# Optimization experiments

Hardware: AMD Instinct MI355X
Metric: run time of the kernel (lower is better)

Reference implementation:

```python
import jax, jax.numpy as jnp
import numpy as np

MU = 0.25  # commitment weight

def setup_inputs() -> dict:
    key = jax.random.key(0)
    k1, k2 = jax.random.split(key)
    x = jax.random.normal(k1, (32, 4096, 32), dtype=jnp.float32)
    codebook = jax.random.normal(k2, (256, 32), dtype=jnp.float32)
    return {"x": x, "codebook": codebook}

def reference(x, codebook):
    B, T, D = x.shape
    K = codebook.shape[0]
    xf = x.reshape(-1, D)  # [N, D]
    d2 = (jnp.sum(xf * xf, axis=-1, keepdims=True)
          + jnp.sum(codebook * codebook, axis=-1)[None, :]
          - 2.0 * (xf @ codebook.T))
    logits = -d2
    probs = jax.nn.softmax(logits, axis=-1)          # [N, K]
    indices = jnp.argmax(logits, axis=-1)            # [N]
    quants_hard = codebook[indices]                  # gather [N, D]
    commitment = jnp.mean((jax.lax.stop_gradient(quants_hard) - xf) ** 2, axis=-1)
    codebook_loss = jnp.mean((quants_hard - jax.lax.stop_gradient(xf)) ** 2, axis=-1)
    loss = codebook_loss + MU * commitment           # [N]
    quants = jax.lax.stop_gradient(quants_hard - xf) + xf  # straight-through
    return (indices.reshape(B, T),
            probs.reshape(B, T, K),
            quants.reshape(B, T, D),
            loss.reshape(B, T))
```

## Files before the change

kernel.cpp:

```cpp
#include <hip/hip_runtime.h>
#include <math.h>

constexpr int D   = 32;
constexpr int K   = 256;
constexpr int RPW = 32;
constexpr int WPB = 4;
constexpr int RPB = RPW * WPB;

typedef __attribute__((ext_vector_type(4))) float fvec4;

template <int CTRL, int RM, int BM>
__device__ __forceinline__ int dpp_i(int id, int v) {
    return __builtin_amdgcn_update_dpp(id, v, CTRL, RM, BM, false);
}

__device__ __forceinline__ float wred_max_f32(float v) {
    const int ID = 0xFF800000;
    v = fmaxf(v, __int_as_float(dpp_i<0x111, 0xF, 0xF>(ID, __float_as_int(v))));
    v = fmaxf(v, __int_as_float(dpp_i<0x112, 0xF, 0xF>(ID, __float_as_int(v))));
    v = fmaxf(v, __int_as_float(dpp_i<0x114, 0xF, 0xF>(ID, __float_as_int(v))));
    v = fmaxf(v, __int_as_float(dpp_i<0x118, 0xF, 0xF>(ID, __float_as_int(v))));
    v = fmaxf(v, __int_as_float(dpp_i<0x142, 0xA, 0xF>(ID, __float_as_int(v))));
    v = fmaxf(v, __int_as_float(dpp_i<0x143, 0xC, 0xF>(ID, __float_as_int(v))));
    return v;
}
__device__ __forceinline__ float wred_add_f32(float v) {
    v = v + __int_as_float(dpp_i<0x111, 0xF, 0xF>(0, __float_as_int(v)));
    v = v + __int_as_float(dpp_i<0x112, 0xF, 0xF>(0, __float_as_int(v)));
    v = v + __int_as_float(dpp_i<0x114, 0xF, 0xF>(0, __float_as_int(v)));
    v = v + __int_as_float(dpp_i<0x118, 0xF, 0xF>(0, __float_as_int(v)));
    v = v + __int_as_float(dpp_i<0x142, 0xA, 0xF>(0, __float_as_int(v)));
    v = v + __int_as_float(dpp_i<0x143, 0xC, 0xF>(0, __float_as_int(v)));
    return v;
}
__device__ __forceinline__ unsigned wred_min_u32(unsigned v) {
    const int ID = (int)0xFFFFFFFF;
    unsigned f;
    f = (unsigned)dpp_i<0x111, 0xF, 0xF>(ID, (int)v); v = v < f ? v : f;
    f = (unsigned)dpp_i<0x112, 0xF, 0xF>(ID, (int)v); v = v < f ? v : f;
    f = (unsigned)dpp_i<0x114, 0xF, 0xF>(ID, (int)v); v = v < f ? v : f;
    f = (unsigned)dpp_i<0x118, 0xF, 0xF>(ID, (int)v); v = v < f ? v : f;
    f = (unsigned)dpp_i<0x142, 0xA, 0xF>(ID, (int)v); v = v < f ? v : f;
    f = (unsigned)dpp_i<0x143, 0xC, 0xF>(ID, (int)v); v = v < f ? v : f;
    return v;
}
__device__ __forceinline__ float bcast63_f32(float v) {
    return __int_as_float(__builtin_amdgcn_readlane(__float_as_int(v), 63));
}

__global__ __launch_bounds__(256, 2) void vq_kernel(
    const float* __restrict__ x,
    const float* __restrict__ cb,
    float* __restrict__ o_idx,
    float* __restrict__ o_probs,
    float* __restrict__ o_quants,
    float* __restrict__ o_loss)
{
    const int tid = threadIdx.x;
    const int l   = tid & 63;
    const int wu  = __builtin_amdgcn_readfirstlane(tid >> 6);
    const int wbase = blockIdx.x * RPB + wu * RPW;

    float cr[4][D];
    #pragma unroll
    for (int j = 0; j < 4; ++j) {
        const float4* cp = reinterpret_cast<const float4*>(cb) + (size_t)(l * 4 + j) * (D / 4);
        #pragma unroll
        for (int i = 0; i < D / 4; ++i) {
            float4 v = cp[i];
            cr[j][4 * i + 0] = v.x; cr[j][4 * i + 1] = v.y;
            cr[j][4 * i + 2] = v.z; cr[j][4 * i + 3] = v.w;
        }
    }
    float ncn[4];
    #pragma unroll
    for (int j = 0; j < 4; ++j) {
        float a0 = 0.f, a1 = 0.f, a2 = 0.f, a3 = 0.f;
        #pragma unroll
        for (int d = 0; d < D; d += 4) {
            a0 += cr[j][d]     * cr[j][d];     a1 += cr[j][d + 1] * cr[j][d + 1];
            a2 += cr[j][d + 2] * cr[j][d + 2]; a3 += cr[j][d + 3] * cr[j][d + 3];
        }
        ncn[j] = -((a0 + a1) + (a2 + a3));
    }

    float xnh;
    {
        const float4* xp = reinterpret_cast<const float4*>(x)
                         + (size_t)(wbase + (l >> 1)) * (D / 4) + (l & 1) * 4;
        float a = 0.f;
        #pragma unroll
        for (int i = 0; i < 4; ++i) {
            float4 v = xp[i];
            a += v.x * v.x + v.y * v.y + v.z * v.z + v.w * v.w;
        }
        float b = __int_as_float(dpp_i<0xB1, 0xF, 0xF>(0, __float_as_int(a)));
        xnh = a + b;
    }

    float    lossv = 0.f, fidx = 0.f;
    unsigned gpark = 0;
    const unsigned codebase = (unsigned)(l * 4);

    for (int g = 0; g < RPW / 8; ++g) {
        float4 vx = reinterpret_cast<const float4*>(x)[(size_t)(wbase + g * 8) * (D / 4) + l];

        #pragma unroll
        for (int rr = 0; rr < 8; ++rr) {
            const int r32 = g * 8 + rr;

            float a0 = 0.f, a1 = 0.f, a2 = 0.f, a3 = 0.f;
            #pragma unroll
            for (int d = 0; d < D; ++d) {
                const int lane = rr * 8 + (d >> 2);
                const int c = d & 3;
                int sb = (c == 0) ? __float_as_int(vx.x)
                       : (c == 1) ? __float_as_int(vx.y)
                       : (c == 2) ? __float_as_int(vx.z)
                       :            __float_as_int(vx.w);
                float xs = __int_as_float(__builtin_amdgcn_readlane(sb, lane));
                a0 = fmaf(cr[0][d], xs, a0);
                a1 = fmaf(cr[1][d], xs, a1);
                a2 = fmaf(cr[2][d], xs, a2);
                a3 = fmaf(cr[3][d], xs, a3);
            }
            float lg0 = fmaf(a0, 2.0f, ncn[0]);
            float lg1 = fmaf(a1, 2.0f, ncn[1]);
            float lg2 = fmaf(a2, 2.0f, ncn[2]);
            float lg3 = fmaf(a3, 2.0f, ncn[3]);

            float m = fmaxf(fmaxf(lg0, lg1), fmaxf(lg2, lg3));
            float gm = bcast63_f32(wred_max_f32(m));

            unsigned c0 = (lg0 == gm) ? (codebase + 0) : 0xFFFFFFFFu;
            unsigned c1 = (lg1 == gm) ? (codebase + 1) : 0xFFFFFFFFu;
            unsigned c2 = (lg2 == gm) ? (codebase + 2) : 0xFFFFFFFFu;
            unsigned c3 = (lg3 == gm) ? (codebase + 3) : 0xFFFFFFFFu;
            unsigned cm = min(min(c0, c1), min(c2, c3));
            unsigned gi = (unsigned)__builtin_amdgcn_readlane((int)wred_min_u32(cm), 63) & 255u;

            float e0 = __expf(lg0 - gm), e1 = __expf(lg1 - gm);
            float e2 = __expf(lg2 - gm), e3 = __expf(lg3 - gm);
            float es = (e0 + e1) + (e2 + e3);
            float ws = wred_add_f32(es);
            float rs = bcast63_f32(__builtin_amdgcn_rcpf(ws));

            fvec4 p4 = { e0 * rs, e1 * rs, e2 * rs, e3 * rs };
            fvec4* pp = reinterpret_cast<fvec4*>(o_probs + (size_t)(wbase + r32) * K) + l;
            __builtin_nontemporal_store(p4, pp);

            bool mA = ((l >> 1) == r32);
            float lv = (xnh - gm) * 0.0390625f;
            lossv = mA ? lv : lossv;
            fidx  = mA ? (float)gi : fidx;
            gpark = ((unsigned)l == (unsigned)r32) ? gi : gpark;
        }
    }

    {
        const int r = l >> 1;
        if ((l & 1) == 0) o_loss[wbase + r] = lossv;
        else              o_idx [wbase + r] = fidx;
    }
    {
        int gsel = __builtin_amdgcn_ds_bpermute((l >> 1) * 4, (int)gpark);
        unsigned gq = (unsigned)gsel & 255u;
        const float4* qs = reinterpret_cast<const float4*>(cb) + (size_t)gq * (D / 4) + (l & 1) * 4;
        float* qd = o_quants + (size_t)(wbase + (l >> 1)) * D + (l & 1) * 16;
        #pragma unroll
        for (int i = 0; i < 4; ++i) {
            float4 v = qs[i];
            fvec4 vv = { v.x, v.y, v.z, v.w };
            __builtin_nontemporal_store(vv, reinterpret_cast<fvec4*>(qd) + i);
        }
    }
}

extern "C" void kernel_launch(void* const* d_in, const int* in_sizes, int n_in,
                              void* d_out, int out_size, void* d_ws, size_t ws_size,
                              hipStream_t stream) {
    const float* x  = (const float*)d_in[0];
    const float* cb = (const float*)d_in[1];
    const int N = in_sizes[0] / D;

    float* out      = (float*)d_out;
    float* o_idx    = out;
    float* o_probs  = o_idx + N;
    float* o_quants = o_probs + (size_t)N * K;
    float* o_loss   = o_quants + (size_t)N * D;

    const int grid = N / RPB;
    vq_kernel<<<grid, 256, 0, stream>>>(x, cb, o_idx, o_probs, o_quants, o_loss);
}
```

Measured before the change: 198.7 us.

## Stage x rows in LDS, use exp2 with prescaled logits, raise occupancy

Each block now copies its 128 input rows into shared memory, and each row's values are read from LDS as broadcast float4 loads instead of through per-element readlane from registers. Logits are prescaled by log2(e) so the softmax can use the hardware exp2 directly, and the loss rescales by ln2. Launch bounds now ask for 3 blocks per CU instead of 2, which tightens the register budget for the 128-float codebook tile each thread keeps. Trade-offs are 16 KB of LDS per block, a block-wide barrier, and a risk of register spills.

```diff
diff --git a/kernel.cpp b/kernel.cpp
--- a/kernel.cpp
+++ b/kernel.cpp
@@ -48,7 +48,7 @@
     return __int_as_float(__builtin_amdgcn_readlane(__float_as_int(v), 63));
 }
 
-__global__ __launch_bounds__(256, 2) void vq_kernel(
+__global__ __launch_bounds__(256, 3) void vq_kernel(
     const float* __restrict__ x,
     const float* __restrict__ cb,
     float* __restrict__ o_idx,
@@ -56,11 +56,22 @@
     float* __restrict__ o_quants,
     float* __restrict__ o_loss)
 {
+    __shared__ float4 xlds[RPB * (D / 4)];
+
     const int tid = threadIdx.x;
     const int l   = tid & 63;
     const int wu  = __builtin_amdgcn_readfirstlane(tid >> 6);
     const int wbase = blockIdx.x * RPB + wu * RPW;
 
+    {
+        const float4* xg = reinterpret_cast<const float4*>(x)
+                         + (size_t)blockIdx.x * RPB * (D / 4);
+        #pragma unroll
+        for (int i = 0; i < 4; ++i) xlds[tid + i * 256] = xg[tid + i * 256];
+    }
+
+    constexpr float SC     = 1.4426950408889634f;
+    constexpr float TWO_SC = 2.8853900817779268f;
     float cr[4][D];
     #pragma unroll
     for (int j = 0; j < 4; ++j) {
@@ -81,7 +92,7 @@
             a0 += cr[j][d]     * cr[j][d];     a1 += cr[j][d + 1] * cr[j][d + 1];
             a2 += cr[j][d + 2] * cr[j][d + 2]; a3 += cr[j][d + 3] * cr[j][d + 3];
         }
-        ncn[j] = -((a0 + a1) + (a2 + a3));
+        ncn[j] = -((a0 + a1) + (a2 + a3)) * SC;
     }
 
     float xnh;
@@ -98,63 +109,60 @@
         xnh = a + b;
     }
 
+    __syncthreads();
+
     float    lossv = 0.f, fidx = 0.f;
     unsigned gpark = 0;
     const unsigned codebase = (unsigned)(l * 4);
-
-    for (int g = 0; g < RPW / 8; ++g) {
-        float4 vx = reinterpret_cast<const float4*>(x)[(size_t)(wbase + g * 8) * (D / 4) + l];
-
-        #pragma unroll
-        for (int rr = 0; rr < 8; ++rr) {
-            const int r32 = g * 8 + rr;
-
-            float a0 = 0.f, a1 = 0.f, a2 = 0.f, a3 = 0.f;
+    const float4* xw4 = xlds + wu * RPW * (D / 4);
+
+    for (int r = 0; r < RPW; ++r) {
+        float a0 = 0.f, a1 = 0.f, a2 = 0.f, a3 = 0.f;
+        #pragma unroll
+        for (int q = 0; q < D / 4; ++q) {
+            float4 xv = xw4[r * (D / 4) + q];
             #pragma unroll
-            for (int d = 0; d < D; ++d) {
-                const int lane = rr * 8 + (d >> 2);
-                const int c = d & 3;
-                int sb = (c == 0) ? __float_as_int(vx.x)
-                       : (c == 1) ? __float_as_int(vx.y)
-                       : (c == 2) ? __float_as_int(vx.z)
-                       :            __float_as_int(vx.w);
-                float xs = __int_as_float(__builtin_amdgcn_readlane(sb, lane));
+            for (int c = 0; c < 4; ++c) {
+                const int d = q * 4 + c;
+                const float xs = (&xv.x)[c];
                 a0 = fmaf(cr[0][d], xs, a0);
                 a1 = fmaf(cr[1][d], xs, a1);
                 a2 = fmaf(cr[2][d], xs, a2);
                 a3 = fmaf(cr[3][d], xs, a3);
             }
-            float lg0 = fmaf(a0, 2.0f, ncn[0]);
-            float lg1 = fmaf(a1, 2.0f, ncn[1]);
-            float lg2 = fmaf(a2, 2.0f, ncn[2]);
-            float lg3 = fmaf(a3, 2.0f, ncn[3]);
-
-            float m = fmaxf(fmaxf(lg0, lg1), fmaxf(lg2, lg3));
-            float gm = bcast63_f32(wred_max_f32(m));
-
-            unsigned c0 = (lg0 == gm) ? (codebase + 0) : 0xFFFFFFFFu;
-            unsigned c1 = (lg1 == gm) ? (codebase + 1) : 0xFFFFFFFFu;
-            unsigned c2 = (lg2 == gm) ? (codebase + 2) : 0xFFFFFFFFu;
-            unsigned c3 = (lg3 == gm) ? (codebase + 3) : 0xFFFFFFFFu;
-            unsigned cm = min(min(c0, c1), min(c2, c3));
-            unsigned gi = (unsigned)__builtin_amdgcn_readlane((int)wred_min_u32(cm), 63) & 255u;
-
-            float e0 = __expf(lg0 - gm), e1 = __expf(lg1 - gm);
-            float e2 = __expf(lg2 - gm), e3 = __expf(lg3 - gm);
-            float es = (e0 + e1) + (e2 + e3);
-            float ws = wred_add_f32(es);
-            float rs = bcast63_f32(__builtin_amdgcn_rcpf(ws));
-
-            fvec4 p4 = { e0 * rs, e1 * rs, e2 * rs, e3 * rs };
-            fvec4* pp = reinterpret_cast<fvec4*>(o_probs + (size_t)(wbase + r32) * K) + l;
-            __builtin_nontemporal_store(p4, pp);
-
-            bool mA = ((l >> 1) == r32);
-            float lv = (xnh - gm) * 0.0390625f;
-            lossv = mA ? lv : lossv;
-            fidx  = mA ? (float)gi : fidx;
-            gpark = ((unsigned)l == (unsigned)r32) ? gi : gpark;
-        }
+        }
+        float slg0 = fmaf(a0, TWO_SC, ncn[0]);
+        float slg1 = fmaf(a1, TWO_SC, ncn[1]);
+        float slg2 = fmaf(a2, TWO_SC, ncn[2]);
+        float slg3 = fmaf(a3, TWO_SC, ncn[3]);
+
+        float m = fmaxf(fmaxf(slg0, slg1), fmaxf(slg2, slg3));
+        float gm = bcast63_f32(wred_max_f32(m));
+
+        unsigned c0 = (slg0 == gm) ? (codebase + 0) : 0xFFFFFFFFu;
+        unsigned c1 = (slg1 == gm) ? (codebase + 1) : 0xFFFFFFFFu;
+        unsigned c2 = (slg2 == gm) ? (codebase + 2) : 0xFFFFFFFFu;
+        unsigned c3 = (slg3 == gm) ? (codebase + 3) : 0xFFFFFFFFu;
+        unsigned cm = min(min(c0, c1), min(c2, c3));
+        unsigned gi = (unsigned)__builtin_amdgcn_readlane((int)wred_min_u32(cm), 63) & 255u;
+
+        float e0 = __builtin_amdgcn_exp2f(slg0 - gm);
+        float e1 = __builtin_amdgcn_exp2f(slg1 - gm);
+        float e2 = __builtin_amdgcn_exp2f(slg2 - gm);
+        float e3 = __builtin_amdgcn_exp2f(slg3 - gm);
+        float es = (e0 + e1) + (e2 + e3);
+        float ws = wred_add_f32(es);
+        float rs = bcast63_f32(__builtin_amdgcn_rcpf(ws));
+
+        fvec4 p4 = { e0 * rs, e1 * rs, e2 * rs, e3 * rs };
+        fvec4* pp = reinterpret_cast<fvec4*>(o_probs + (size_t)(wbase + r) * K) + l;
+        __builtin_nontemporal_store(p4, pp);
+
+        bool mA = ((l >> 1) == r);
+        float lv = (xnh - gm * 0.6931471805599453f) * 0.0390625f;
+        lossv = mA ? lv : lossv;
+        fidx  = mA ? (float)gi : fidx;
+        gpark = ((unsigned)l == (unsigned)r) ? gi : gpark;
     }
 
     {
```

New measurement: 194.1 us. 2.3% less time.
